# Kernel tuning notes

Measured on AMD Instinct MI355X. Metric: run time of the kernel, lower is better.

The kernel has to match this reference:

```python
import jax, jax.numpy as jnp
import numpy as np

B, C, L, H, W = 8, 64, 32, 64, 64

def setup_inputs() -> dict:
    key = jax.random.key(0)
    k1, k2, k3, k4, k5 = jax.random.split(key, 5)
    inpt = jax.random.normal(k1, (B, C, L, H, W), dtype=jnp.float32)
    # 1x1x1 conv kernels collapse to per-channel vectors
    theta_w = jax.random.normal(k2, (C,), dtype=jnp.float32) * 0.1  # Conv3d(c,1,1) weight
    g_w = jax.random.normal(k3, (C,), dtype=jnp.float32) * 0.1      # Conv3d(c,1,1) weight
    h_w = jax.random.normal(k4, (C,), dtype=jnp.float32) * 0.1      # Conv3d(1,c,1) weight
    h_b = jax.random.normal(k5, (C,), dtype=jnp.float32) * 0.1      # Conv3d(1,c,1) bias
    return {"inpt": inpt, "theta_w": theta_w, "g_w": g_w, "h_w": h_w, "h_b": h_b}

def reference(inpt, theta_w, g_w, h_w, h_b):
    b, c, l, h, w = inpt.shape
    # theta/g: 1x1x1 convs c->1 == channel contraction
    t = jnp.einsum('bclhw,c->blhw', inpt, theta_w).reshape(b, -1)  # (b, N)
    g = jnp.einsum('bclhw,c->blhw', inpt, g_w).reshape(b, -1)      # (b, N)
    # outer product t[b,1,N]*g[b,N,1] followed by AvgPool1d(N) over last axis
    # == g scaled by mean(t); skip the O(N^2) intermediate entirely
    mt = jnp.mean(t, axis=1, keepdims=True)                        # (b, 1)
    x = (g * mt).reshape(b, 1, l, h, w)
    # h: 1x1x1 conv 1->c with bias
    y = x * h_w[None, :, None, None, None] + h_b[None, :, None, None, None]
    return inpt + y
```

## Files before the change

kernel.cpp:

```cpp
#include <hip/hip_runtime.h>

#define BB 8
#define CC 64
#define NSP 131072
#define QPB 8
#define NPART (BB * CC * QPB)

__global__ __launch_bounds__(256) void k1_sum(
    const float* __restrict__ inpt, float* __restrict__ partials)
{
    int blk = blockIdx.x;
    int bc = blk >> 3, q = blk & 7;
    const float4* base = reinterpret_cast<const float4*>(inpt)
                         + (((size_t)bc) << 15) + (q << 12);
    float4 s4 = make_float4(0.f, 0.f, 0.f, 0.f);
    #pragma unroll
    for (int i = 0; i < 16; ++i) {
        float4 x = base[i * 256 + threadIdx.x];
        s4.x += x.x; s4.y += x.y; s4.z += x.z; s4.w += x.w;
    }
    float s = (s4.x + s4.y) + (s4.z + s4.w);
    #pragma unroll
    for (int off = 32; off > 0; off >>= 1) s += __shfl_down(s, off);
    __shared__ float red[4];
    int wid = threadIdx.x >> 6;
    if ((threadIdx.x & 63) == 0) red[wid] = s;
    __syncthreads();
    if (threadIdx.x == 0) partials[blk] = (red[0] + red[1]) + (red[2] + red[3]);
}

__global__ __launch_bounds__(512) void k2_mt(
    const float* __restrict__ partials, const float* __restrict__ theta_w,
    float* __restrict__ mt)
{
    int b = threadIdx.x >> 6;
    int c = threadIdx.x & 63;
    const float* p = partials + (((b << 6) | c) << 3);
    float v = ((p[0] + p[1]) + (p[2] + p[3])) + ((p[4] + p[5]) + (p[6] + p[7]));
    v *= theta_w[c];
    #pragma unroll
    for (int off = 32; off > 0; off >>= 1) v += __shfl_down(v, off);
    if (c == 0) mt[b] = v * (1.0f / (float)NSP);
}

__global__ __launch_bounds__(256) void k3_fused(
    const float* __restrict__ inpt, const float* __restrict__ g_w,
    const float* __restrict__ mt, const float* __restrict__ h_w,
    const float* __restrict__ h_b, float* __restrict__ out)
{
    int rblk = (int)gridDim.x - 1 - (int)blockIdx.x;
    size_t idx = (size_t)rblk * 256 + threadIdx.x;
    int b = (int)(idx >> 17);
    size_t n = idx & (NSP - 1);
    const float* base = inpt + ((((size_t)b) << 6) << 17) + n;

    float vals[CC];
    float gacc = 0.f;
    #pragma unroll
    for (int c = 0; c < CC; ++c) {
        vals[c] = base[((size_t)c) << 17];
        gacc = fmaf(vals[c], g_w[c], gacc);
    }
    float s = gacc * mt[b];
    float* obase = out + ((((size_t)b) << 6) << 17) + n;
    #pragma unroll
    for (int c = 0; c < CC; ++c) {
        float o = fmaf(s, h_w[c], vals[c] + h_b[c]);
        __builtin_nontemporal_store(o, obase + (((size_t)c) << 17));
    }
}

extern "C" void kernel_launch(void* const* d_in, const int* in_sizes, int n_in,
                              void* d_out, int out_size, void* d_ws, size_t ws_size,
                              hipStream_t stream)
{
    const float* inpt    = (const float*)d_in[0];
    const float* theta_w = (const float*)d_in[1];
    const float* g_w     = (const float*)d_in[2];
    const float* h_w     = (const float*)d_in[3];
    const float* h_b     = (const float*)d_in[4];
    float* out = (float*)d_out;

    char* ws = (char*)d_ws;
    float* partials = (float*)ws;
    float* mt       = (float*)(ws + NPART * sizeof(float));

    hipLaunchKernelGGL(k1_sum, dim3(NPART), dim3(256), 0, stream,
                       inpt, partials);
    hipLaunchKernelGGL(k2_mt, dim3(1), dim3(512), 0, stream,
                       partials, theta_w, mt);
    hipLaunchKernelGGL(k3_fused, dim3((BB * NSP) / 256), dim3(256), 0, stream,
                       inpt, g_w, mt, h_w, h_b, out);
}
```

Before: 127.8 us.

## Pipeline per-batch reduction with previous batch's fused output across launches

```diff
diff --git a/kernel.cpp b/kernel.cpp
--- a/kernel.cpp
+++ b/kernel.cpp
@@ -3,70 +3,68 @@
 #define BB 8
 #define CC 64
 #define NSP 131072
-#define QPB 8
-#define NPART (BB * CC * QPB)
+#define PPB 512
 
-__global__ __launch_bounds__(256) void k1_sum(
-    const float* __restrict__ inpt, float* __restrict__ partials)
+__global__ __launch_bounds__(256) void k_pipe(
+    const float* __restrict__ inpt, const float* __restrict__ theta_w,
+    const float* __restrict__ g_w, const float* __restrict__ h_w,
+    const float* __restrict__ h_b, float* __restrict__ out,
+    float* __restrict__ partials, int b_k1, int b_k3)
 {
-    int blk = blockIdx.x;
-    int bc = blk >> 3, q = blk & 7;
-    const float4* base = reinterpret_cast<const float4*>(inpt)
-                         + (((size_t)bc) << 15) + (q << 12);
-    float4 s4 = make_float4(0.f, 0.f, 0.f, 0.f);
-    #pragma unroll
-    for (int i = 0; i < 16; ++i) {
-        float4 x = base[i * 256 + threadIdx.x];
-        s4.x += x.x; s4.y += x.y; s4.z += x.z; s4.w += x.w;
-    }
-    float s = (s4.x + s4.y) + (s4.z + s4.w);
-    #pragma unroll
-    for (int off = 32; off > 0; off >>= 1) s += __shfl_down(s, off);
-    __shared__ float red[4];
-    int wid = threadIdx.x >> 6;
-    if ((threadIdx.x & 63) == 0) red[wid] = s;
-    __syncthreads();
-    if (threadIdx.x == 0) partials[blk] = (red[0] + red[1]) + (red[2] + red[3]);
-}
+    if (blockIdx.x < PPB) {
+        if (b_k1 >= BB) return;
+        int blk = blockIdx.x;
+        int bc  = (b_k1 << 6) + (blk >> 3);
+        int q   = blk & 7;
+        const float4* base = reinterpret_cast<const float4*>(inpt)
+                             + (((size_t)bc) << 15) + ((size_t)q << 12);
+        float4 s4 = make_float4(0.f, 0.f, 0.f, 0.f);
+        #pragma unroll
+        for (int i = 0; i < 16; ++i) {
+            float4 x = base[i * 256 + threadIdx.x];
+            s4.x += x.x; s4.y += x.y; s4.z += x.z; s4.w += x.w;
+        }
+        float s = (s4.x + s4.y) + (s4.z + s4.w);
+        #pragma unroll
+        for (int off = 32; off > 0; off >>= 1) s += __shfl_down(s, off);
+        __shared__ float red[4];
+        int wid = threadIdx.x >> 6;
+        if ((threadIdx.x & 63) == 0) red[wid] = s;
+        __syncthreads();
+        if (threadIdx.x == 0)
+            partials[(b_k1 << 9) + blk] = (red[0] + red[1]) + (red[2] + red[3]);
+    } else {
+        if (b_k3 < 0) return;
+        int blk  = (int)blockIdx.x - PPB;
+        int lane = threadIdx.x & 63;
 
-__global__ __launch_bounds__(512) void k2_mt(
-    const float* __restrict__ partials, const float* __restrict__ theta_w,
-    float* __restrict__ mt)
-{
-    int b = threadIdx.x >> 6;
-    int c = threadIdx.x & 63;
-    const float* p = partials + (((b << 6) | c) << 3);
-    float v = ((p[0] + p[1]) + (p[2] + p[3])) + ((p[4] + p[5]) + (p[6] + p[7]));
-    v *= theta_w[c];
-    #pragma unroll
-    for (int off = 32; off > 0; off >>= 1) v += __shfl_down(v, off);
-    if (c == 0) mt[b] = v * (1.0f / (float)NSP);
-}
+        const float* p = partials + (b_k3 << 9);
+        float v = 0.f;
+        #pragma unroll
+        for (int i = 0; i < 8; ++i) {
+            int idx = i * 64 + lane;
+            v = fmaf(p[idx], theta_w[idx >> 3], v);
+        }
+        #pragma unroll
+        for (int off = 32; off > 0; off >>= 1) v += __shfl_down(v, off);
+        float mt = __shfl(v, 0) * (1.0f / (float)NSP);
 
-__global__ __launch_bounds__(256) void k3_fused(
-    const float* __restrict__ inpt, const float* __restrict__ g_w,
-    const float* __restrict__ mt, const float* __restrict__ h_w,
-    const float* __restrict__ h_b, float* __restrict__ out)
-{
-    int rblk = (int)gridDim.x - 1 - (int)blockIdx.x;
-    size_t idx = (size_t)rblk * 256 + threadIdx.x;
-    int b = (int)(idx >> 17);
-    size_t n = idx & (NSP - 1);
-    const float* base = inpt + ((((size_t)b) << 6) << 17) + n;
-
-    float vals[CC];
-    float gacc = 0.f;
-    #pragma unroll
-    for (int c = 0; c < CC; ++c) {
-        vals[c] = base[((size_t)c) << 17];
-        gacc = fmaf(vals[c], g_w[c], gacc);
-    }
-    float s = gacc * mt[b];
-    float* obase = out + ((((size_t)b) << 6) << 17) + n;
-    #pragma unroll
-    for (int c = 0; c < CC; ++c) {
-        float o = fmaf(s, h_w[c], vals[c] + h_b[c]);
-        __builtin_nontemporal_store(o, obase + (((size_t)c) << 17));
+        size_t n = ((size_t)blk << 8) + threadIdx.x;
+        const float* base  = inpt + (((size_t)b_k3) << 23) + n;
+        float vals[CC];
+        float gacc = 0.f;
+        #pragma unroll
+        for (int c = 0; c < CC; ++c) {
+            vals[c] = base[((size_t)c) << 17];
+            gacc = fmaf(vals[c], g_w[c], gacc);
+        }
+        float sc = gacc * mt;
+        float* obase = out + (((size_t)b_k3) << 23) + n;
+        #pragma unroll
+        for (int c = 0; c < CC; ++c) {
+            float o = fmaf(sc, h_w[c], vals[c] + h_b[c]);
+            __builtin_nontemporal_store(o, obase + (((size_t)c) << 17));
+        }
     }
 }
 
@@ -81,14 +79,11 @@
     const float* h_b     = (const float*)d_in[4];
     float* out = (float*)d_out;
 
-    char* ws = (char*)d_ws;
-    float* partials = (float*)ws;
-    float* mt       = (float*)(ws + NPART * sizeof(float));
+    float* partials = (float*)d_ws;
 
-    hipLaunchKernelGGL(k1_sum, dim3(NPART), dim3(256), 0, stream,
-                       inpt, partials);
-    hipLaunchKernelGGL(k2_mt, dim3(1), dim3(512), 0, stream,
-                       partials, theta_w, mt);
-    hipLaunchKernelGGL(k3_fused, dim3((BB * NSP) / 256), dim3(256), 0, stream,
-                       inpt, g_w, mt, h_w, h_b, out);
+    for (int s = 0; s <= BB; ++s) {
+        hipLaunchKernelGGL(k_pipe, dim3(2 * PPB), dim3(256), 0, stream,
+                           inpt, theta_w, g_w, h_w, h_b, out, partials,
+                           s, s - 1);
+    }
 }
```

Result: slower. 150.9 us (+18.0%).
